# Optimization experiments

Hardware: AMD Instinct MI355X
Metric: run time of the kernel (lower is better)

The kernel has to match this reference:

```python
import jax, jax.numpy as jnp
import numpy as np
import math

D_KEY = 64
SCALE = math.sqrt(D_KEY)
INF = 1e10  # finite stand-in for the original INF constant
CAUSAL = True
DIAG = False


def setup_inputs() -> dict:
    key = jax.random.key(0)
    kq, kk, kv = jax.random.split(key, 3)
    B, L, D = 16, 2048, D_KEY
    return {
        "query": jax.random.normal(kq, (B, L, D), dtype=jnp.float32),
        "key": jax.random.normal(kk, (B, L, D), dtype=jnp.float32),
        "value": jax.random.normal(kv, (B, L, D), dtype=jnp.float32),
    }


def reference(query, key, value):
    # scores: [B, Lq, Lk]
    scores = jnp.einsum("bqd,bkd->bqk", query, key)
    L = key.shape[1]
    if CAUSAL:
        # subtract INF above the diagonal (strict upper triangle), as in torch triu(1)
        tri = jnp.triu(jnp.full((L, L), INF, dtype=scores.dtype), k=1)
        scores = scores - tri[None, :, :]
    if DIAG:
        # original scatters -INF onto the diagonal along dim 1
        diag_mask = jnp.eye(L, dtype=bool)
        scores = jnp.where(diag_mask[None, :, :], -INF, scores)
    # softmax over keys after scaling; dropout with p=0.0 is identity
    attn = jax.nn.softmax(scores / SCALE, axis=-1)
    return jnp.einsum("bqk,bkd->bqd", attn, value)
```

## Files before the change

kernel.cpp:

```cpp
#include <hip/hip_runtime.h>

typedef __bf16 bf16_t;
typedef __bf16 bf16x4 __attribute__((ext_vector_type(4)));
typedef __bf16 bf16x8 __attribute__((ext_vector_type(8)));
typedef float  f32x4  __attribute__((ext_vector_type(4)));

#define B_SZ  16
#define L_SEQ 2048
#define D_H   64
#define QB    128
#define KB    128
#define NT128 16
#define TILE_HW (KB * D_H)
#define IMG_ELEMS ((size_t)B_SZ * NT128 * TILE_HW)

#define QSCALE 0.18033688011112043f

#define GLD_LDS16(g, l) __builtin_amdgcn_global_load_lds(                       \
    (const __attribute__((address_space(1))) void*)(g),                         \
    (__attribute__((address_space(3))) void*)(l), 16, 0, 0)

__global__ __launch_bounds__(256)
void preproc_kernel(const float* __restrict__ Kg, const float* __restrict__ Vg,
                    bf16_t* __restrict__ Kimg, bf16_t* __restrict__ Vimg)
{
    const int kt = blockIdx.x, b = blockIdx.y, z = blockIdx.z;
    const int t  = threadIdx.x;
    const size_t src = (size_t)b * L_SEQ * D_H + (size_t)kt * KB * D_H;
    bf16_t* ko = Kimg + (size_t)(b * NT128 + kt) * TILE_HW;
    bf16_t* vo = Vimg + (size_t)(b * NT128 + kt) * TILE_HW;

    {
        const int u = z * 256 + t, r = u >> 3, ch = u & 7;
        const float* p = Kg + src + r * 64 + ch * 8;
        const f32x4 a = *reinterpret_cast<const f32x4*>(p);
        const f32x4 c = *reinterpret_cast<const f32x4*>(p + 4);
        bf16x8 kk;
#pragma unroll
        for (int j = 0; j < 4; ++j) { kk[j] = (bf16_t)a[j]; kk[4 + j] = (bf16_t)c[j]; }
        *reinterpret_cast<bf16x8*>(&ko[r * 64 + ((ch ^ (r & 7)) << 3)]) = kk;
    }

    {
        const int d = t & 63, pc = (t >> 6) + z * 4;
        bf16x8 vv;
#pragma unroll
        for (int pw = 0; pw < 8; ++pw) {
            const int pos = pc * 8 + pw;
            const int vkb = ((pos >> 3) & 3) | (((pos >> 2) & 1) << 2) | (((pos >> 5) & 3) << 3);
            const int k   = (vkb << 2) | (pos & 3);
            vv[pw] = (bf16_t)Vg[src + (size_t)k * 64 + d];
        }
        *reinterpret_cast<bf16x8*>(&vo[d * 128 + ((pc ^ (d & 7)) << 3)]) = vv;
    }
}

__global__ __launch_bounds__(512, 1)
void attn_split_kernel(const float* __restrict__ Qg, float* __restrict__ Og,
                       const bf16_t* __restrict__ Kimg, const bf16_t* __restrict__ Vimg,
                       float* __restrict__ Opart, float* __restrict__ MLb)
{
    const int lin  = blockIdx.x;
    const int xcd  = lin & 7;
    const int b    = xcd * 2 + ((lin >> 3) & 1);
    const int p    = (lin >> 4) & 7;
    const int role = lin >> 7;

    const int nktL = 16 - p;
    const int nktS = p + 1;
    const int cnt1 = role ? (nktL - 9) : 9;
    const int cnt2 = role ? nktS : 0;
    const int total = cnt1 + cnt2;
    const int ktoff = role ? 9 : 0;

    const int tid  = threadIdx.x;
    const int wave = tid >> 6;
    const int lane = tid & 63;
    const int lg   = lane >> 4;
    const int lc   = lane & 15;
    const int lc7  = lc & 7;

    __shared__ __align__(16) bf16_t K_lds[2][TILE_HW];
    __shared__ __align__(16) bf16_t Vt_lds[2][TILE_HW];

    const size_t bbase = (size_t)b * L_SEQ * D_H;
    const bf16_t* kimg = Kimg + (size_t)b * NT128 * TILE_HW;
    const bf16_t* vimg = Vimg + (size_t)b * NT128 * TILE_HW;

    auto stage = [&](int kt, int buf) {
        const bf16_t* ks = kimg + (size_t)kt * TILE_HW;
        const bf16_t* vs = vimg + (size_t)kt * TILE_HW;
#pragma unroll
        for (int i = 0; i < 2; ++i) {
            const int c = wave * 2 + i;
            GLD_LDS16(ks + c * 512 + lane * 8, &K_lds[buf][c * 512]);
            GLD_LDS16(vs + c * 512 + lane * 8, &Vt_lds[buf][c * 512]);
        }
    };

    bf16x8 qa[2];
    auto loadQ = [&](int qt_) -> int {
        const int qr = qt_ * QB + wave * 16 + lc;
#pragma unroll
        for (int h = 0; h < 2; ++h) {
            const float* qp = Qg + bbase + (size_t)qr * D_H + h * 32 + lg * 8;
            const f32x4 f0 = *reinterpret_cast<const f32x4*>(qp);
            const f32x4 f1 = *reinterpret_cast<const f32x4*>(qp + 4);
            bf16x8 a;
#pragma unroll
            for (int j = 0; j < 4; ++j) { a[j] = (bf16_t)(f0[j] * QSCALE); a[4 + j] = (bf16_t)(f1[j] * QSCALE); }
            qa[h] = a;
        }
        return qr;
    };

    int qt = 15 - p, nktCur = nktL;
    int qrow = loadQ(qt);

    f32x4 o[4];
#pragma unroll
    for (int dt = 0; dt < 4; ++dt) o[dt] = (f32x4){0.f, 0.f, 0.f, 0.f};
    float m = -1e30f, l = 0.f;

    auto writePartialL = [&]() {
        float lr = l;
        lr += __shfl_xor(lr, 16);
        lr += __shfl_xor(lr, 32);
        const int slot = (b * 8 + p) * 2 + role;
        float* ob = Opart + (size_t)slot * (QB * D_H);
        const int qL = wave * 16 + lc;
#pragma unroll
        for (int dt = 0; dt < 4; ++dt)
            *reinterpret_cast<f32x4*>(&ob[qL * 64 + dt * 16 + lg * 4]) = o[dt];
        if (lg == 0) { MLb[slot * 256 + qL] = m; MLb[slot * 256 + 128 + qL] = lr; }
    };

    auto seqKt = [&](int j) { return j < cnt1 ? ktoff + j : j - cnt1; };

    stage(seqKt(0), 0);
    __syncthreads();
    int cur = 0;
    for (int j = 0; j < total; ++j) {
        if (role && j == cnt1) {
            writePartialL();
            qt = p; nktCur = nktS; qrow = loadQ(qt);
#pragma unroll
            for (int dt = 0; dt < 4; ++dt) o[dt] = (f32x4){0.f, 0.f, 0.f, 0.f};
            m = -1e30f; l = 0.f;
        }
        const int kt  = seqKt(j);
        const int kb0 = kt * KB;
        if (j + 1 < total) stage(seqKt(j + 1), cur ^ 1);

        f32x4 sc[8];
        __builtin_amdgcn_s_setprio(1);
#pragma unroll
        for (int n = 0; n < 8; ++n) {
            f32x4 acc = (f32x4){0.f, 0.f, 0.f, 0.f};
#pragma unroll
            for (int h = 0; h < 2; ++h) {
                const int hw = (n * 16 + lc) * 64 + ((((h << 2) | lg) ^ lc7) << 3);
                const bf16x8 kkb = *reinterpret_cast<const bf16x8*>(&K_lds[cur][hw]);
                acc = __builtin_amdgcn_mfma_f32_16x16x32_bf16(kkb, qa[h], acc, 0, 0, 0);
            }
            sc[n] = acc;
        }
        __builtin_amdgcn_s_setprio(0);
        if (kt == nktCur - 1) {
#pragma unroll
            for (int n = 0; n < 8; ++n)
#pragma unroll
                for (int r = 0; r < 4; ++r)
                    if (kb0 + n * 16 + lg * 4 + r > qrow) sc[n][r] = -1e30f;
        }

        float mxp = fmaxf(fmaxf(sc[0][0], sc[0][1]), fmaxf(sc[0][2], sc[0][3]));
#pragma unroll
        for (int n = 1; n < 8; ++n)
            mxp = fmaxf(mxp, fmaxf(fmaxf(sc[n][0], sc[n][1]), fmaxf(sc[n][2], sc[n][3])));
        if (!__all(mxp <= m + 8.0f)) {
            float mx = mxp;
            mx = fmaxf(mx, __shfl_xor(mx, 16));
            mx = fmaxf(mx, __shfl_xor(mx, 32));
            const float mn = fmaxf(m, mx);
            const float alpha = exp2f(m - mn);
            m = mn;
            l *= alpha;
#pragma unroll
            for (int dt = 0; dt < 4; ++dt)
#pragma unroll
                for (int r = 0; r < 4; ++r) o[dt][r] *= alpha;
        }
        bf16x8 w[4];
        float rs = 0.f;
#pragma unroll
        for (int n = 0; n < 8; ++n) {
            const float p0 = exp2f(sc[n][0] - m), p1 = exp2f(sc[n][1] - m);
            const float p2 = exp2f(sc[n][2] - m), p3 = exp2f(sc[n][3] - m);
            rs += (p0 + p1) + (p2 + p3);
            const int wi = n >> 1, off = (n & 1) * 4;
            w[wi][off + 0] = (bf16_t)p0; w[wi][off + 1] = (bf16_t)p1;
            w[wi][off + 2] = (bf16_t)p2; w[wi][off + 3] = (bf16_t)p3;
        }
        l += rs;

        __builtin_amdgcn_s_setprio(1);
#pragma unroll
        for (int ks = 0; ks < 4; ++ks) {
#pragma unroll
            for (int dt = 0; dt < 4; ++dt) {
                const int hw = (dt * 16 + lc) * 128 + ((((ks << 2) | lg) ^ lc7) << 3);
                const bf16x8 vb = *reinterpret_cast<const bf16x8*>(&Vt_lds[cur][hw]);
                o[dt] = __builtin_amdgcn_mfma_f32_16x16x32_bf16(vb, w[ks], o[dt], 0, 0, 0);
            }
        }
        __builtin_amdgcn_s_setprio(0);

        __syncthreads();
        cur ^= 1;
    }

    if (role == 0) {
        writePartialL();
    } else {
        float lr = l;
        lr += __shfl_xor(lr, 16);
        lr += __shfl_xor(lr, 32);
        const float inv = 1.0f / lr;
#pragma unroll
        for (int dt = 0; dt < 4; ++dt) {
            f32x4 val = { o[dt][0] * inv, o[dt][1] * inv, o[dt][2] * inv, o[dt][3] * inv };
            *reinterpret_cast<f32x4*>(Og + bbase + (size_t)qrow * D_H + dt * 16 + lg * 4) = val;
        }
    }
}

__global__ __launch_bounds__(256)
void merge_kernel(const float* __restrict__ Opart, const float* __restrict__ MLb,
                  float* __restrict__ Og)
{
    const int blk     = blockIdx.x;
    const int pairIdx = blk >> 2;
    const int sub     = blk & 3;
    const int b  = pairIdx >> 3, p = pairIdx & 7;
    const int qt = 15 - p;
    const int t  = threadIdx.x;
    const int q  = sub * 32 + (t >> 3);
    const int dc = (t & 7) * 8;

    const int slot0 = pairIdx * 2, slot1 = slot0 + 1;
    const float m0 = MLb[slot0 * 256 + q], l0 = MLb[slot0 * 256 + 128 + q];
    const float m1 = MLb[slot1 * 256 + q], l1 = MLb[slot1 * 256 + 128 + q];
    const float mt = fmaxf(m0, m1);
    const float a0 = exp2f(m0 - mt), a1 = exp2f(m1 - mt);
    const float inv = 1.0f / (l0 * a0 + l1 * a1);

    const float* o0 = Opart + (size_t)slot0 * (QB * D_H) + q * 64 + dc;
    const float* o1 = Opart + (size_t)slot1 * (QB * D_H) + q * 64 + dc;
    float* og = Og + (size_t)b * L_SEQ * D_H + (size_t)(qt * QB + q) * D_H + dc;
#pragma unroll
    for (int i = 0; i < 2; ++i) {
        const f32x4 v0 = *reinterpret_cast<const f32x4*>(o0 + i * 4);
        const f32x4 v1 = *reinterpret_cast<const f32x4*>(o1 + i * 4);
        f32x4 r;
#pragma unroll
        for (int k = 0; k < 4; ++k) r[k] = (v0[k] * a0 + v1[k] * a1) * inv;
        *reinterpret_cast<f32x4*>(og + i * 4) = r;
    }
}

__global__ __launch_bounds__(256, 2)
void attn_fwd_fb(const float* __restrict__ Qg, const float* __restrict__ Kg,
                 const float* __restrict__ Vg, float* __restrict__ Og)
{
    const int lin  = blockIdx.x;
    const int xcd  = lin & 7;
    const int slot = lin >> 3;
    const int half = slot >> 5;
    const int qi   = slot & 31;
    const int b    = xcd * 2 + half;
    const int qt   = half ? qi : (31 - qi);

    const int tid  = threadIdx.x;
    const int lane = tid & 63;
    const int lg   = lane >> 4;
    const int lc   = lane & 15;
    const int lc7  = lc & 7;

    __shared__ __align__(16) bf16_t K_lds[2][KB * D_H];
    __shared__ __align__(16) bf16_t Vt_lds[2][D_H * KB];

    const size_t bbase = (size_t)b * L_SEQ * D_H;
    const int qrow = qt * 64 + (tid >> 6) * 16 + lc;
    bf16x8 qa[2];
#pragma unroll
    for (int h = 0; h < 2; ++h) {
        const float* qp = Qg + bbase + (size_t)qrow * D_H + h * 32 + lg * 8;
        const f32x4 f0 = *reinterpret_cast<const f32x4*>(qp);
        const f32x4 f1 = *reinterpret_cast<const f32x4*>(qp + 4);
        bf16x8 a;
#pragma unroll
        for (int j = 0; j < 4; ++j) { a[j] = (bf16_t)(f0[j] * QSCALE); a[4 + j] = (bf16_t)(f1[j] * QSCALE); }
        qa[h] = a;
    }
    f32x4 o[4];
#pragma unroll
    for (int dt = 0; dt < 4; ++dt) o[dt] = (f32x4){0.f, 0.f, 0.f, 0.f};
    float m = -1e30f, l = 0.f;
    const int nkt = (qt + 2) >> 1;
    const int vkb  = tid & 31;
    const int vdg  = tid >> 5;
    const int vpos = ((vkb >> 3) << 5) + ((vkb & 3) << 3) + (((vkb >> 2) & 1) << 2);
    f32x4 kreg[8], vreg[8];

    auto issueK = [&](int kt) {
        const int kbase = kt * KB;
#pragma unroll
        for (int i = 0; i < 4; ++i) {
            const int u = i * 256 + tid;
            const int r = u >> 3, ch = u & 7;
            const float* p = Kg + bbase + (size_t)(kbase + r) * D_H + ch * 8;
            kreg[2 * i]     = *reinterpret_cast<const f32x4*>(p);
            kreg[2 * i + 1] = *reinterpret_cast<const f32x4*>(p + 4);
        }
    };
    auto issueV = [&](int kt) {
        const int kbase = kt * KB;
#pragma unroll
        for (int d2 = 0; d2 < 2; ++d2)
#pragma unroll
            for (int i = 0; i < 4; ++i)
                vreg[d2 * 4 + i] = *reinterpret_cast<const f32x4*>(
                    Vg + bbase + (size_t)(kbase + vkb * 4 + i) * D_H + (vdg + d2 * 8) * 4);
    };
    auto writeK = [&](int buf) {
#pragma unroll
        for (int i = 0; i < 4; ++i) {
            const int u = i * 256 + tid;
            const int r = u >> 3, ch = u & 7;
            bf16x8 kk;
#pragma unroll
            for (int j = 0; j < 4; ++j) { kk[j] = (bf16_t)kreg[2 * i][j]; kk[4 + j] = (bf16_t)kreg[2 * i + 1][j]; }
            *reinterpret_cast<bf16x8*>(&K_lds[buf][r * 64 + ((ch ^ (r & 7)) << 3)]) = kk;
        }
    };
    auto writeV = [&](int buf) {
#pragma unroll
        for (int d2 = 0; d2 < 2; ++d2) {
            const int db = vdg + d2 * 8;
#pragma unroll
            for (int j = 0; j < 4; ++j) {
                const int d = db * 4 + j;
                bf16x4 cj = { (bf16_t)vreg[d2 * 4 + 0][j], (bf16_t)vreg[d2 * 4 + 1][j],
                              (bf16_t)vreg[d2 * 4 + 2][j], (bf16_t)vreg[d2 * 4 + 3][j] };
                const int hw = d * 128 + (((vpos >> 3) ^ (d & 7)) << 3) + (vpos & 7);
                *reinterpret_cast<bf16x4*>(&Vt_lds[buf][hw]) = cj;
            }
        }
    };

    issueK(0); issueV(0); writeK(0); writeV(0);
    __syncthreads();
    int cur = 0;
    for (int kt = 0; kt < nkt; ++kt) {
        const bool last = (kt == nkt - 1);
        const int kbase = kt * KB;
        if (!last) issueK(kt + 1);
        f32x4 sc[8];
#pragma unroll
        for (int n = 0; n < 8; ++n) {
            f32x4 acc = (f32x4){0.f, 0.f, 0.f, 0.f};
#pragma unroll
            for (int h = 0; h < 2; ++h) {
                const int hw = (n * 16 + lc) * 64 + ((((h << 2) | lg) ^ lc7) << 3);
                const bf16x8 kkb = *reinterpret_cast<const bf16x8*>(&K_lds[cur][hw]);
                acc = __builtin_amdgcn_mfma_f32_16x16x32_bf16(kkb, qa[h], acc, 0, 0, 0);
            }
            sc[n] = acc;
        }
        if (!last) issueV(kt + 1);
        if (last) {
#pragma unroll
            for (int n = 0; n < 8; ++n)
#pragma unroll
                for (int r = 0; r < 4; ++r)
                    if (kbase + n * 16 + lg * 4 + r > qrow) sc[n][r] = -1e30f;
        }
        float mxp = fmaxf(fmaxf(sc[0][0], sc[0][1]), fmaxf(sc[0][2], sc[0][3]));
#pragma unroll
        for (int n = 1; n < 8; ++n)
            mxp = fmaxf(mxp, fmaxf(fmaxf(sc[n][0], sc[n][1]), fmaxf(sc[n][2], sc[n][3])));
        if (!__all(mxp <= m + 8.0f)) {
            float mx = mxp;
            mx = fmaxf(mx, __shfl_xor(mx, 16));
            mx = fmaxf(mx, __shfl_xor(mx, 32));
            const float mn = fmaxf(m, mx);
            const float alpha = exp2f(m - mn);
            m = mn; l *= alpha;
#pragma unroll
            for (int dt = 0; dt < 4; ++dt)
#pragma unroll
                for (int r = 0; r < 4; ++r) o[dt][r] *= alpha;
        }
        bf16x8 w[4];
        float rs = 0.f;
#pragma unroll
        for (int n = 0; n < 8; ++n) {
            const float p0 = exp2f(sc[n][0] - m), p1 = exp2f(sc[n][1] - m);
            const float p2 = exp2f(sc[n][2] - m), p3 = exp2f(sc[n][3] - m);
            rs += (p0 + p1) + (p2 + p3);
            const int wi = n >> 1, off = (n & 1) * 4;
            w[wi][off + 0] = (bf16_t)p0; w[wi][off + 1] = (bf16_t)p1;
            w[wi][off + 2] = (bf16_t)p2; w[wi][off + 3] = (bf16_t)p3;
        }
        l += rs;
        if (!last) writeK(cur ^ 1);
#pragma unroll
        for (int ks = 0; ks < 4; ++ks) {
#pragma unroll
            for (int dt = 0; dt < 4; ++dt) {
                const int hw = (dt * 16 + lc) * 128 + ((((ks << 2) | lg) ^ lc7) << 3);
                const bf16x8 vb = *reinterpret_cast<const bf16x8*>(&Vt_lds[cur][hw]);
                o[dt] = __builtin_amdgcn_mfma_f32_16x16x32_bf16(vb, w[ks], o[dt], 0, 0, 0);
            }
        }
        if (!last) writeV(cur ^ 1);
        __syncthreads();
        cur ^= 1;
    }
    float lr = l;
    lr += __shfl_xor(lr, 16);
    lr += __shfl_xor(lr, 32);
    const float inv = 1.0f / lr;
#pragma unroll
    for (int dt = 0; dt < 4; ++dt) {
        f32x4 val = { o[dt][0] * inv, o[dt][1] * inv, o[dt][2] * inv, o[dt][3] * inv };
        *reinterpret_cast<f32x4*>(Og + bbase + (size_t)qrow * D_H + dt * 16 + lg * 4) = val;
    }
}

extern "C" void kernel_launch(void* const* d_in, const int* in_sizes, int n_in,
                              void* d_out, int out_size, void* d_ws, size_t ws_size,
                              hipStream_t stream)
{
    const float* Q = (const float*)d_in[0];
    const float* K = (const float*)d_in[1];
    const float* V = (const float*)d_in[2];
    float* O = (float*)d_out;

    const size_t img_bytes = 2 * IMG_ELEMS * sizeof(bf16_t);
    const size_t opart_fl  = (size_t)B_SZ * 8 * 2 * (QB * D_H);
    const size_t ml_fl     = (size_t)B_SZ * 8 * 2 * 256;
    const size_t need = img_bytes + (opart_fl + ml_fl) * sizeof(float);

    if (ws_size >= need) {
        bf16_t* Kimg  = (bf16_t*)d_ws;
        bf16_t* Vimg  = Kimg + IMG_ELEMS;
        float*  Opart = (float*)((char*)d_ws + img_bytes);
        float*  MLb   = Opart + opart_fl;
        preproc_kernel<<<dim3(NT128, B_SZ, 4), dim3(256), 0, stream>>>(K, V, Kimg, Vimg);
        attn_split_kernel<<<dim3(256), dim3(512), 0, stream>>>(Q, O, Kimg, Vimg, Opart, MLb);
        merge_kernel<<<dim3(512), dim3(256), 0, stream>>>(Opart, MLb, O);
    } else {
        attn_fwd_fb<<<dim3(512), dim3(256), 0, stream>>>(Q, K, V, O);
    }
}
```

Before: 39.63 us.

## Split paired causal q-tiles into four KV chunks per block with 4-way merge

```diff
diff --git a/kernel.cpp b/kernel.cpp
--- a/kernel.cpp
+++ b/kernel.cpp
@@ -40,7 +40,6 @@
         for (int j = 0; j < 4; ++j) { kk[j] = (bf16_t)a[j]; kk[4 + j] = (bf16_t)c[j]; }
         *reinterpret_cast<bf16x8*>(&ko[r * 64 + ((ch ^ (r & 7)) << 3)]) = kk;
     }
-
     {
         const int d = t & 63, pc = (t >> 6) + z * 4;
         bf16x8 vv;
@@ -55,23 +54,27 @@
     }
 }
 
-__global__ __launch_bounds__(512, 1)
-void attn_split_kernel(const float* __restrict__ Qg, float* __restrict__ Og,
-                       const bf16_t* __restrict__ Kimg, const bf16_t* __restrict__ Vimg,
-                       float* __restrict__ Opart, float* __restrict__ MLb)
+__global__ __launch_bounds__(512, 4)
+void attn_split4_kernel(const float* __restrict__ Qg, float* __restrict__ Og,
+                        const bf16_t* __restrict__ Kimg, const bf16_t* __restrict__ Vimg,
+                        float* __restrict__ Opart, float* __restrict__ MLb)
 {
     const int lin  = blockIdx.x;
     const int xcd  = lin & 7;
     const int b    = xcd * 2 + ((lin >> 3) & 1);
     const int p    = (lin >> 4) & 7;
-    const int role = lin >> 7;
+    const int role = (lin >> 7) & 3;
+    const int pair = b * 8 + p;
 
     const int nktL = 16 - p;
-    const int nktS = p + 1;
-    const int cnt1 = role ? (nktL - 9) : 9;
-    const int cnt2 = role ? nktS : 0;
-    const int total = cnt1 + cnt2;
-    const int ktoff = role ? 9 : 0;
+    const int OFFS[5] = {0, 5, 9, 13, 17};
+    const int posStart = OFFS[role];
+    const int total    = OFFS[role + 1] - posStart;
+    int cnt1 = nktL - posStart;
+    cnt1 = cnt1 < 0 ? 0 : (cnt1 > total ? total : cnt1);
+
+    const int slotL = (pair * 4 + role) * 2;
+    const int slotS = slotL + 1;
 
     const int tid  = threadIdx.x;
     const int wave = tid >> 6;
@@ -87,6 +90,8 @@
     const bf16_t* kimg = Kimg + (size_t)b * NT128 * TILE_HW;
     const bf16_t* vimg = Vimg + (size_t)b * NT128 * TILE_HW;
 
+    auto posToKt = [&](int j) { const int pos = posStart + j; return pos < nktL ? pos : pos - nktL; };
+
     auto stage = [&](int kt, int buf) {
         const bf16_t* ks = kimg + (size_t)kt * TILE_HW;
         const bf16_t* vs = vimg + (size_t)kt * TILE_HW;
@@ -114,7 +119,7 @@
         return qr;
     };
 
-    int qt = 15 - p, nktCur = nktL;
+    int qt   = (cnt1 > 0) ? (15 - p) : p;
     int qrow = loadQ(qt);
 
     f32x4 o[4];
@@ -122,11 +127,10 @@
     for (int dt = 0; dt < 4; ++dt) o[dt] = (f32x4){0.f, 0.f, 0.f, 0.f};
     float m = -1e30f, l = 0.f;
 
-    auto writePartialL = [&]() {
+    auto writePartial = [&](int slot) {
         float lr = l;
         lr += __shfl_xor(lr, 16);
         lr += __shfl_xor(lr, 32);
-        const int slot = (b * 8 + p) * 2 + role;
         float* ob = Opart + (size_t)slot * (QB * D_H);
         const int qL = wave * 16 + lc;
 #pragma unroll
@@ -134,23 +138,27 @@
             *reinterpret_cast<f32x4*>(&ob[qL * 64 + dt * 16 + lg * 4]) = o[dt];
         if (lg == 0) { MLb[slot * 256 + qL] = m; MLb[slot * 256 + 128 + qL] = lr; }
     };
-
-    auto seqKt = [&](int j) { return j < cnt1 ? ktoff + j : j - cnt1; };
-
-    stage(seqKt(0), 0);
+    auto writeEmpty = [&](int slot) {
+        const int qL = wave * 16 + lc;
+        if (lg == 0) { MLb[slot * 256 + qL] = -1e30f; MLb[slot * 256 + 128 + qL] = 0.f; }
+    };
+
+    stage(posToKt(0), 0);
     __syncthreads();
     int cur = 0;
+
     for (int j = 0; j < total; ++j) {
-        if (role && j == cnt1) {
-            writePartialL();
-            qt = p; nktCur = nktS; qrow = loadQ(qt);
+        if (cnt1 > 0 && cnt1 < total && j == cnt1) {
+            writePartial(slotL);
+            qt = p; qrow = loadQ(qt);
 #pragma unroll
             for (int dt = 0; dt < 4; ++dt) o[dt] = (f32x4){0.f, 0.f, 0.f, 0.f};
             m = -1e30f; l = 0.f;
         }
-        const int kt  = seqKt(j);
+        const int pos = posStart + j;
+        const int kt  = pos < nktL ? pos : pos - nktL;
         const int kb0 = kt * KB;
-        if (j + 1 < total) stage(seqKt(j + 1), cur ^ 1);
+        if (j + 1 < total) stage(posToKt(j + 1), cur ^ 1);
 
         f32x4 sc[8];
         __builtin_amdgcn_s_setprio(1);
@@ -166,7 +174,9 @@
             sc[n] = acc;
         }
         __builtin_amdgcn_s_setprio(0);
-        if (kt == nktCur - 1) {
+
+        const bool diag = (pos == nktL - 1) || (pos == 16);
+        if (diag) {
 #pragma unroll
             for (int n = 0; n < 8; ++n)
 #pragma unroll
@@ -220,52 +230,67 @@
         cur ^= 1;
     }
 
-    if (role == 0) {
-        writePartialL();
+    if (cnt1 == total) {
+        writePartial(slotL);
+        writeEmpty(slotS);
+    } else if (cnt1 == 0) {
+        writeEmpty(slotL);
+        writePartial(slotS);
     } else {
-        float lr = l;
-        lr += __shfl_xor(lr, 16);
-        lr += __shfl_xor(lr, 32);
-        const float inv = 1.0f / lr;
-#pragma unroll
-        for (int dt = 0; dt < 4; ++dt) {
-            f32x4 val = { o[dt][0] * inv, o[dt][1] * inv, o[dt][2] * inv, o[dt][3] * inv };
-            *reinterpret_cast<f32x4*>(Og + bbase + (size_t)qrow * D_H + dt * 16 + lg * 4) = val;
-        }
+        writePartial(slotS);
     }
 }
 
 __global__ __launch_bounds__(256)
-void merge_kernel(const float* __restrict__ Opart, const float* __restrict__ MLb,
-                  float* __restrict__ Og)
+void merge4_kernel(const float* __restrict__ Opart, const float* __restrict__ MLb,
+                   float* __restrict__ Og)
 {
     const int blk     = blockIdx.x;
-    const int pairIdx = blk >> 2;
-    const int sub     = blk & 3;
-    const int b  = pairIdx >> 3, p = pairIdx & 7;
-    const int qt = 15 - p;
+    const int tileIdx = blk >> 1;
+    const int sub     = blk & 1;
+    const int pair    = tileIdx >> 1;
+    const int type    = tileIdx & 1;
+    const int b  = pair >> 3, p = pair & 7;
+    const int qt = type ? p : (15 - p);
     const int t  = threadIdx.x;
-    const int q  = sub * 32 + (t >> 3);
-    const int dc = (t & 7) * 8;
-
-    const int slot0 = pairIdx * 2, slot1 = slot0 + 1;
-    const float m0 = MLb[slot0 * 256 + q], l0 = MLb[slot0 * 256 + 128 + q];
-    const float m1 = MLb[slot1 * 256 + q], l1 = MLb[slot1 * 256 + 128 + q];
-    const float mt = fmaxf(m0, m1);
-    const float a0 = exp2f(m0 - mt), a1 = exp2f(m1 - mt);
-    const float inv = 1.0f / (l0 * a0 + l1 * a1);
-
-    const float* o0 = Opart + (size_t)slot0 * (QB * D_H) + q * 64 + dc;
-    const float* o1 = Opart + (size_t)slot1 * (QB * D_H) + q * 64 + dc;
+    const int q  = sub * 64 + (t >> 2);
+    const int dc = (t & 3) * 16;
+
+    float mv[4], lv[4];
+#pragma unroll
+    for (int r = 0; r < 4; ++r) {
+        const int slot = (pair * 4 + r) * 2 + type;
+        mv[r] = MLb[slot * 256 + q];
+        lv[r] = MLb[slot * 256 + 128 + q];
+    }
+    const float mt = fmaxf(fmaxf(mv[0], mv[1]), fmaxf(mv[2], mv[3]));
+    float wv[4], den = 0.f;
+#pragma unroll
+    for (int r = 0; r < 4; ++r) { wv[r] = exp2f(mv[r] - mt); den += lv[r] * wv[r]; }
+    const float inv = 1.0f / den;
+
+    f32x4 acc[4];
+#pragma unroll
+    for (int i = 0; i < 4; ++i) acc[i] = (f32x4){0.f, 0.f, 0.f, 0.f};
+#pragma unroll
+    for (int r = 0; r < 4; ++r) {
+        if (lv[r] != 0.0f) {
+            const float* orp = Opart + (size_t)((pair * 4 + r) * 2 + type) * (QB * D_H) + q * 64 + dc;
+#pragma unroll
+            for (int i = 0; i < 4; ++i) {
+                const f32x4 v = *reinterpret_cast<const f32x4*>(orp + i * 4);
+#pragma unroll
+                for (int k2 = 0; k2 < 4; ++k2) acc[i][k2] += v[k2] * wv[r];
+            }
+        }
+    }
     float* og = Og + (size_t)b * L_SEQ * D_H + (size_t)(qt * QB + q) * D_H + dc;
 #pragma unroll
-    for (int i = 0; i < 2; ++i) {
-        const f32x4 v0 = *reinterpret_cast<const f32x4*>(o0 + i * 4);
-        const f32x4 v1 = *reinterpret_cast<const f32x4*>(o1 + i * 4);
-        f32x4 r;
-#pragma unroll
-        for (int k = 0; k < 4; ++k) r[k] = (v0[k] * a0 + v1[k] * a1) * inv;
-        *reinterpret_cast<f32x4*>(og + i * 4) = r;
+    for (int i = 0; i < 4; ++i) {
+        f32x4 rr;
+#pragma unroll
+        for (int k2 = 0; k2 < 4; ++k2) rr[k2] = acc[i][k2] * inv;
+        *reinterpret_cast<f32x4*>(og + i * 4) = rr;
     }
 }
 
@@ -449,8 +474,8 @@
     float* O = (float*)d_out;
 
     const size_t img_bytes = 2 * IMG_ELEMS * sizeof(bf16_t);
-    const size_t opart_fl  = (size_t)B_SZ * 8 * 2 * (QB * D_H);
-    const size_t ml_fl     = (size_t)B_SZ * 8 * 2 * 256;
+    const size_t opart_fl  = (size_t)1024 * (QB * D_H);
+    const size_t ml_fl     = (size_t)1024 * 256;
     const size_t need = img_bytes + (opart_fl + ml_fl) * sizeof(float);
 
     if (ws_size >= need) {
@@ -459,8 +484,8 @@
         float*  Opart = (float*)((char*)d_ws + img_bytes);
         float*  MLb   = Opart + opart_fl;
         preproc_kernel<<<dim3(NT128, B_SZ, 4), dim3(256), 0, stream>>>(K, V, Kimg, Vimg);
-        attn_split_kernel<<<dim3(256), dim3(512), 0, stream>>>(Q, O, Kimg, Vimg, Opart, MLb);
-        merge_kernel<<<dim3(512), dim3(256), 0, stream>>>(Opart, MLb, O);
+        attn_split4_kernel<<<dim3(512), dim3(512), 0, stream>>>(Q, O, Kimg, Vimg, Opart, MLb);
+        merge4_kernel<<<dim3(512), dim3(256), 0, stream>>>(Opart, MLb, O);
     } else {
         attn_fwd_fb<<<dim3(512), dim3(256), 0, stream>>>(Q, K, V, O);
     }
```

Result: slower. 42.56 us (+7.4%).
